# Performance work log

Measured on AMD Instinct MI355X. Metric: run time of the kernel, lower is better.

Reference implementation:

```python
import jax, jax.numpy as jnp
import numpy as np

HEADS = 8
FEATURE = 512
COMPUTE = 256
SEQ = 512
BATCH = 64


def setup_inputs() -> dict:
    key = jax.random.key(0)
    ks = jax.random.split(key, 10)
    d1 = jax.random.normal(ks[0], (BATCH, FEATURE), dtype=jnp.float32)
    d2 = jax.random.normal(ks[1], (SEQ, BATCH, FEATURE), dtype=jnp.float32)
    # linear1: Linear(FEATURE -> COMPUTE) + ReLU
    w1 = jax.random.normal(ks[2], (FEATURE, COMPUTE), dtype=jnp.float32) * (1.0 / np.sqrt(FEATURE))
    b1 = jnp.zeros((COMPUTE,), dtype=jnp.float32)
    # per-head score params, stacked: ws[i] is [2C, C], ps[i] is [C, 1]
    W = jax.random.normal(ks[3], (HEADS, 2 * COMPUTE, COMPUTE), dtype=jnp.float32)
    P = jax.random.normal(ks[4], (HEADS, COMPUTE), dtype=jnp.float32)
    # value projection weight_v: [FEATURE, COMPUTE]
    wv = jax.random.normal(ks[5], (FEATURE, COMPUTE), dtype=jnp.float32)
    # cc: Linear(COMPUTE*HEADS -> 128) + ReLU
    wcc = jax.random.normal(ks[6], (COMPUTE * HEADS, 128), dtype=jnp.float32) * (1.0 / np.sqrt(COMPUTE * HEADS))
    bcc = jnp.zeros((128,), dtype=jnp.float32)
    return {"d1": d1, "d2": d2, "w1": w1, "b1": b1, "W": W, "P": P,
            "wv": wv, "wcc": wcc, "bcc": bcc, "d2_size": SEQ}


def reference(d1, d2, w1, b1, W, P, wv, wcc, bcc, d2_size):
    S, B, F = d2.shape
    # linear1 on flattened d2 rows -> [S*B, C]
    d3 = jax.nn.relu(d2.reshape(-1, F) @ w1 + b1)
    # linear1 on d1, tiled S times along batch axis -> [S*B, C]
    d4 = jax.nn.relu(d1 @ w1 + b1)            # [B, C]
    d4 = jnp.tile(d4, (S, 1))                  # [S*B, C]
    d5 = jnp.concatenate([d3, d4], axis=1).reshape(S, B, -1)  # [S, B, 2C]
    # value path: tanh(d2 @ weight_v) -> [B, S, C]
    tv = jnp.tanh(jnp.einsum('sbf,fc->sbc', d2, wv)).transpose(1, 0, 2)
    # all heads batched: us = tanh(d5 @ W_h) -> [H, S, B, C]
    us = jnp.tanh(jnp.einsum('sbd,hdc->hsbc', d5, W))
    atts = jnp.einsum('hsbc,hc->hbs', us, P)   # [H, B, S]
    scores = jax.nn.softmax(atts, axis=-1)     # softmax over sequence
    vs = jnp.einsum('hbs,bsc->hbc', scores, tv)  # weighted sum over S -> [H, B, C]
    # torch.cat(vs, dim=1): head-major concat -> [B, H*C]
    vs = vs.transpose(1, 0, 2).reshape(B, -1)
    return jax.nn.relu(vs @ wcc + bcc)         # [B, 128]
```

## Files before the change

kernel.cpp:

```cpp
#include <hip/hip_runtime.h>
#include <cstddef>
#include <cstdint>

#define HH 8
#define FF 512
#define CC 256
#define SS 512
#define BB 64
#define SB (SS*BB)

typedef __attribute__((ext_vector_type(4))) float f32x4;
typedef __attribute__((ext_vector_type(8))) short bf16x8;

typedef __attribute__((address_space(1))) unsigned int gu32_t;
typedef __attribute__((address_space(3))) unsigned int lu32_t;

__device__ __forceinline__ void gld16(const void* gp, void* lp) {
    __builtin_amdgcn_global_load_lds((gu32_t*)gp, (lu32_t*)lp, 16, 0, 0);
}

__device__ __forceinline__ float fast_tanh(float x) {
    float e = __expf(2.0f * x);
    return 1.0f - 2.0f / (e + 1.0f);
}
__device__ __forceinline__ float relu_f(float x) { return fmaxf(x, 0.0f); }

__device__ __forceinline__ unsigned short f2bf(float x) {
    unsigned u = __float_as_uint(x);
    unsigned r = u + 0x7FFFu + ((u >> 16) & 1u);
    return (unsigned short)(r >> 16);
}
__device__ __forceinline__ float bf2f(unsigned short h) {
    return __uint_as_float(((unsigned)h) << 16);
}


__global__ __launch_bounds__(256) void p_prep(
    const float* __restrict__ w1, const float* __restrict__ wv,
    const float* __restrict__ W, const float* __restrict__ d1,
    const float* __restrict__ b1,
    unsigned short* __restrict__ w1ts, unsigned short* __restrict__ wvts,
    unsigned short* __restrict__ Wts, float* __restrict__ d4)
{
    __shared__ float T[64][65];
    __shared__ float As[16][68];
    __shared__ float Bs[16][68];
    const int tid = threadIdx.x;
    const int bid = blockIdx.x;
    if (bid < 192) {
        const float* src;
        unsigned short* dst;
        int kt64, nt;
        if (bid < 64) {
            int m = bid >> 5;
            int t = bid & 31;
            kt64 = t >> 2; nt = t & 3;
            src = m ? wv : w1;
            dst = m ? wvts : w1ts;
        } else {
            int t = bid - 64;
            int h = t >> 4; int tt = t & 15;
            kt64 = tt >> 2; nt = tt & 3;
            src = W + (size_t)h * 2 * CC * CC;
            dst = Wts + (size_t)h * 8 * CC * 64;
        }
        const int k0 = kt64 * 64, n0 = nt * 64;
        #pragma unroll
        for (int jj = 0; jj < 4; ++jj) {
            int i = (tid >> 4) + jj * 16;
            int j = (tid & 15) * 4;
            float4 v = *(const float4*)(src + (size_t)(k0 + i) * CC + n0 + j);
            T[i][j] = v.x; T[i][j+1] = v.y; T[i][j+2] = v.z; T[i][j+3] = v.w;
        }
        __syncthreads();
        {
            const int n_local = tid & 63;
            const int kg = (tid >> 6) * 16;
            const int n_abs = n0 + n_local;
            const int sxn = n_abs & 7;
            #pragma unroll
            for (int j = 0; j < 2; ++j) {
                const int kbase = kg + j * 8;
                const int k_abs = k0 + kbase;
                const int kt = k_abs >> 5;
                const int g = (k_abs >> 3) & 3;
                bf16x8 hv8, lv8;
                #pragma unroll
                for (int q = 0; q < 8; ++q) {
                    float x = T[kbase + q][n_local];
                    unsigned short hx = f2bf(x);
                    hv8[q] = (short)hx;
                    lv8[q] = (short)f2bf(x - bf2f(hx));
                }
                size_t rowo = ((size_t)kt * CC + n_abs) * 64;
                *(bf16x8*)(dst + rowo + (size_t)((2*g + 0) ^ sxn) * 8) = hv8;
                *(bf16x8*)(dst + rowo + (size_t)((2*g + 1) ^ sxn) * 8) = lv8;
            }
        }
    } else {
        const int n0 = (bid - 192) * 64;
        const int tx = tid & 15, ty = tid >> 4;
        const int lm = tid >> 2, lk4 = (tid & 3) * 4;
        const int bk = tid >> 4, bn4 = (tid & 15) * 4;
        float acc[4][4] = {};
        for (int k0 = 0; k0 < FF; k0 += 16) {
            float4 a = *(const float4*)(d1 + (size_t)lm * FF + k0 + lk4);
            As[lk4+0][lm] = a.x; As[lk4+1][lm] = a.y;
            As[lk4+2][lm] = a.z; As[lk4+3][lm] = a.w;
            *(float4*)&Bs[bk][bn4] = *(const float4*)(w1 + (size_t)(k0+bk)*CC + n0 + bn4);
            __syncthreads();
            #pragma unroll
            for (int kk = 0; kk < 16; ++kk) {
                float4 a4 = *(const float4*)&As[kk][ty*4];
                float4 b4 = *(const float4*)&Bs[kk][tx*4];
                float av[4] = {a4.x, a4.y, a4.z, a4.w};
                float bv[4] = {b4.x, b4.y, b4.z, b4.w};
                #pragma unroll
                for (int i = 0; i < 4; ++i)
                    #pragma unroll
                    for (int j = 0; j < 4; ++j)
                        acc[i][j] = fmaf(av[i], bv[j], acc[i][j]);
            }
            __syncthreads();
        }
        #pragma unroll
        for (int i = 0; i < 4; ++i) {
            int row = ty*4 + i;
            #pragma unroll
            for (int j = 0; j < 4; ++j)
                d4[(size_t)row*CC + n0 + tx*4 + j] = relu_f(acc[i][j] + b1[n0 + tx*4 + j]);
        }
    }
}

__global__ __launch_bounds__(256, 2) void k1_main(
    const float* __restrict__ d2,
    const unsigned short* __restrict__ w1ts, const unsigned short* __restrict__ wvts,
    const float* __restrict__ b1,
    const float* __restrict__ d4, const float* __restrict__ W,
    unsigned short* __restrict__ d3s, unsigned short* __restrict__ tv,
    float* __restrict__ e4)
{
    __shared__ __align__(16) unsigned short SH[24576];
    unsigned short* const Abuf = SH;
    unsigned short* const Bbuf = SH + 8192;

    const int tid = threadIdx.x;
    const int bid = blockIdx.x;

    if (bid >= 512) {
        float (*As)[68] = (float(*)[68])&SH[0];
        float (*Bs)[68] = (float(*)[68])&SH[8192];
        const int idx = bid - 512;
        const int n0 = (idx & 3) * 64;
        const int h  = idx >> 2;
        const float* Wh = W + ((size_t)h * 2 * CC + CC) * CC;
        const int tx = tid & 15, ty = tid >> 4;
        const int lm = tid >> 2, lk4 = (tid & 3) * 4;
        const int bk = tid >> 4, bn4 = (tid & 15) * 4;
        float acc[4][4] = {};
        for (int k0 = 0; k0 < CC; k0 += 16) {
            float4 a = *(const float4*)(d4 + (size_t)lm * CC + k0 + lk4);
            As[lk4+0][lm] = a.x; As[lk4+1][lm] = a.y;
            As[lk4+2][lm] = a.z; As[lk4+3][lm] = a.w;
            *(float4*)&Bs[bk][bn4] = *(const float4*)(Wh + (size_t)(k0+bk)*CC + n0 + bn4);
            __syncthreads();
            #pragma unroll
            for (int kk = 0; kk < 16; ++kk) {
                float4 a4 = *(const float4*)&As[kk][ty*4];
                float4 b4 = *(const float4*)&Bs[kk][tx*4];
                float av[4] = {a4.x, a4.y, a4.z, a4.w};
                float bv[4] = {b4.x, b4.y, b4.z, b4.w};
                #pragma unroll
                for (int i = 0; i < 4; ++i)
                    #pragma unroll
                    for (int j = 0; j < 4; ++j)
                        acc[i][j] = fmaf(av[i], bv[j], acc[i][j]);
            }
            __syncthreads();
        }
        #pragma unroll
        for (int i = 0; i < 4; ++i) {
            int b = ty*4 + i;
            #pragma unroll
            for (int j = 0; j < 4; ++j)
                e4[((size_t)h*BB + b)*CC + n0 + tx*4 + j] = acc[i][j];
        }
        return;
    }

    const int cxcd = bid & 7;
    const int jd   = bid >> 3;
    const int path = jd & 1;
    const int xb   = (jd >> 1) * 8 + cxcd;
    const int r0   = xb * 128;
    const int lane = tid & 63, w = tid >> 6;
    const int rowgrp = w & 1, colgrp = w >> 1;
    const int cb = lane & 15, quad = lane >> 4;
    const unsigned short* BT = path ? wvts : w1ts;

    f32x4 acc[4][8];
    f32x4 zero = {0.0f, 0.0f, 0.0f, 0.0f};
    #pragma unroll
    for (int rt = 0; rt < 4; ++rt)
        #pragma unroll
        for (int ct = 0; ct < 8; ++ct) acc[rt][ct] = zero;

    const int ar = tid >> 1, ak = (tid & 1) * 16;
    const int arx = ar & 7;
    const int g0 = ak >> 3;
    const int phi = (2 * quad) ^ (cb & 7);

    for (int k0 = 0; k0 < FF; k0 += 32) {
        const int kt = k0 >> 5;
        {
            const unsigned short* Bsrc = BT + (size_t)kt * (CC * 64);
            #pragma unroll
            for (int i = 0; i < 8; ++i) {
                int chunk = i * 4 + w;
                gld16(Bsrc + (size_t)chunk * 512 + lane * 8, &Bbuf[chunk * 512]);
            }
        }
        {
            const float* s = d2 + (size_t)(r0 + ar) * FF + k0 + ak;
            float v[16];
            *(float4*)&v[0]  = *(const float4*)(s);
            *(float4*)&v[4]  = *(const float4*)(s + 4);
            *(float4*)&v[8]  = *(const float4*)(s + 8);
            *(float4*)&v[12] = *(const float4*)(s + 12);
            bf16x8 vh0, vh1, vl0, vl1;
            #pragma unroll
            for (int j = 0; j < 8; ++j) {
                unsigned short h = f2bf(v[j]);
                vh0[j] = (short)h; vl0[j] = (short)f2bf(v[j] - bf2f(h));
                unsigned short h2 = f2bf(v[j+8]);
                vh1[j] = (short)h2; vl1[j] = (short)f2bf(v[j+8] - bf2f(h2));
            }
            unsigned short* Ar = &Abuf[ar * 64];
            *(bf16x8*)&Ar[((2*g0 + 0) ^ arx) * 8] = vh0;
            *(bf16x8*)&Ar[((2*g0 + 1) ^ arx) * 8] = vl0;
            *(bf16x8*)&Ar[((2*g0 + 2) ^ arx) * 8] = vh1;
            *(bf16x8*)&Ar[((2*g0 + 3) ^ arx) * 8] = vl1;
        }
        __syncthreads();
        bf16x8 ahf[4], alf[4];
        #pragma unroll
        for (int rt = 0; rt < 4; ++rt) {
            const unsigned short* Arow = &Abuf[(rowgrp*64 + rt*16 + cb) * 64];
            ahf[rt] = *(const bf16x8*)&Arow[phi * 8];
            alf[rt] = *(const bf16x8*)&Arow[(phi ^ 1) * 8];
        }
        #pragma unroll
        for (int ct = 0; ct < 8; ++ct) {
            const unsigned short* Brow = &Bbuf[(colgrp*128 + ct*16 + cb) * 64];
            bf16x8 bh = *(const bf16x8*)&Brow[phi * 8];
            bf16x8 bl = *(const bf16x8*)&Brow[(phi ^ 1) * 8];
            #pragma unroll
            for (int rt = 0; rt < 4; ++rt) {
                acc[rt][ct] = __builtin_amdgcn_mfma_f32_16x16x32_bf16(ahf[rt], bh, acc[rt][ct], 0, 0, 0);
                acc[rt][ct] = __builtin_amdgcn_mfma_f32_16x16x32_bf16(ahf[rt], bl, acc[rt][ct], 0, 0, 0);
                acc[rt][ct] = __builtin_amdgcn_mfma_f32_16x16x32_bf16(alf[rt], bh, acc[rt][ct], 0, 0, 0);
            }
        }
        __syncthreads();
    }

    if (path == 0) {
        float bias[8];
        #pragma unroll
        for (int ct = 0; ct < 8; ++ct) bias[ct] = b1[colgrp*128 + ct*16 + cb];
        unsigned short* Lp = SH + colgrp * 9216;
        #pragma unroll
        for (int it = 0; it < 4; ++it) {
            __syncthreads();
            #pragma unroll
            for (int rt = 0; rt < 4; ++rt)
                #pragma unroll
                for (int r = 0; r < 4; ++r) {
                    int row = rowgrp*64 + rt*16 + quad*4 + r;
                    int sx = row & 7;
                    #pragma unroll
                    for (int t = 0; t < 2; ++t) {
                        float val = relu_f(acc[rt][2*it + t][r] + bias[2*it + t]);
                        unsigned short hx = f2bf(val);
                        unsigned short lx = f2bf(val - bf2f(hx));
                        int cl = t*16 + cb;
                        int g = cl >> 3, c7 = cl & 7;
                        Lp[row*72 + (((2*g + 0) ^ sx) << 3) + c7] = hx;
                        Lp[row*72 + (((2*g + 1) ^ sx) << 3) + c7] = lx;
                    }
                }
            __syncthreads();
            #pragma unroll
            for (int q = 0; q < 8; ++q) {
                int idx = q*256 + tid;
                int pp  = idx >> 10;
                int rc  = idx & 1023;
                int row = rc >> 3;
                int ch  = rc & 7;
                bf16x8 v = *(const bf16x8*)&SH[pp*9216 + row*72 + ch*8];
                unsigned short* dst = d3s + ((size_t)(pp*4 + it) * SB + r0 + row) * 64;
                *(bf16x8*)&dst[ch*8] = v;
            }
        }
    } else {
        unsigned short* Lp = SH + colgrp * 6144;
        #pragma unroll
        for (int it = 0; it < 4; ++it) {
            __syncthreads();
            #pragma unroll
            for (int rt = 0; rt < 4; ++rt)
                #pragma unroll
                for (int r = 0; r < 4; ++r) {
                    int row = rowgrp*64 + rt*16 + quad*4 + r;
                    #pragma unroll
                    for (int t = 0; t < 2; ++t) {
                        int cl = t*16 + cb;
                        Lp[row*48 + cl] = f2bf(fast_tanh(acc[rt][2*it + t][r]));
                    }
                }
            __syncthreads();
            #pragma unroll
            for (int q = 0; q < 4; ++q) {
                int idx = q*256 + tid;
                int pp  = idx >> 9;
                int rc  = idx & 511;
                int row = rc >> 2;
                int ch  = rc & 3;
                bf16x8 v = *(const bf16x8*)&SH[pp*6144 + row*48 + ch*8];
                unsigned short* dst = tv + (size_t)(r0 + row) * CC + (pp*4 + it)*32;
                *(bf16x8*)&dst[ch*8] = v;
            }
        }
    }
}

__global__ __launch_bounds__(256, 2) void k3_atts(
    const unsigned short* __restrict__ d3s, const unsigned short* __restrict__ Wts,
    const float* __restrict__ e4, const float* __restrict__ P,
    float* __restrict__ atts)
{
    __shared__ __align__(16) unsigned short Abuf[128 * 64];
    __shared__ __align__(16) unsigned short Bbuf[256 * 64];
    float (*red)[128] = (float(*)[128])&Abuf[0];

    const int tid = threadIdx.x;
    const int lane = tid & 63, w = tid >> 6;
    const int bid = blockIdx.x;
    const int cxcd = bid & 7;
    const int jj   = bid >> 3;
    const int h    = jj & 7;
    const int xb   = (jj >> 3) * 8 + cxcd;
    const int r0   = xb * 128;
    const int rowgrp = w & 1, colgrp = w >> 1;
    const int cb = lane & 15, quad = lane >> 4;
    const int phi = (2 * quad) ^ (cb & 7);

    const unsigned short* Wh = Wts + (size_t)h * (8 * CC * 64);

    f32x4 acc[4][8];
    f32x4 zero = {0.0f, 0.0f, 0.0f, 0.0f};
    #pragma unroll
    for (int rt = 0; rt < 4; ++rt)
        #pragma unroll
        for (int ct = 0; ct < 8; ++ct) acc[rt][ct] = zero;

    for (int kt = 0; kt < 8; ++kt) {
        {
            const unsigned short* Asrc = d3s + ((size_t)kt * SB + r0) * 64;
            #pragma unroll
            for (int i = 0; i < 4; ++i) {
                int chunk = i * 4 + w;
                gld16(Asrc + (size_t)chunk * 512 + lane * 8, &Abuf[chunk * 512]);
            }
        }
        {
            const unsigned short* Bsrc = Wh + (size_t)kt * (CC * 64);
            #pragma unroll
            for (int i = 0; i < 8; ++i) {
                int chunk = i * 4 + w;
                gld16(Bsrc + (size_t)chunk * 512 + lane * 8, &Bbuf[chunk * 512]);
            }
        }
        __syncthreads();
        bf16x8 ahf[4], alf[4];
        #pragma unroll
        for (int rt = 0; rt < 4; ++rt) {
            const unsigned short* Arow = &Abuf[(rowgrp*64 + rt*16 + cb) * 64];
            ahf[rt] = *(const bf16x8*)&Arow[phi * 8];
            alf[rt] = *(const bf16x8*)&Arow[(phi ^ 1) * 8];
        }
        #pragma unroll
        for (int ct = 0; ct < 8; ++ct) {
            const unsigned short* Brow = &Bbuf[(colgrp*128 + ct*16 + cb) * 64];
            bf16x8 bh = *(const bf16x8*)&Brow[phi * 8];
            bf16x8 bl = *(const bf16x8*)&Brow[(phi ^ 1) * 8];
            #pragma unroll
            for (int rt = 0; rt < 4; ++rt) {
                acc[rt][ct] = __builtin_amdgcn_mfma_f32_16x16x32_bf16(ahf[rt], bh, acc[rt][ct], 0, 0, 0);
                acc[rt][ct] = __builtin_amdgcn_mfma_f32_16x16x32_bf16(ahf[rt], bl, acc[rt][ct], 0, 0, 0);
                acc[rt][ct] = __builtin_amdgcn_mfma_f32_16x16x32_bf16(alf[rt], bh, acc[rt][ct], 0, 0, 0);
            }
        }
        __syncthreads();
    }
    float Pv[8];
    #pragma unroll
    for (int ct = 0; ct < 8; ++ct) Pv[ct] = P[(size_t)h * CC + colgrp*128 + ct*16 + cb];
    #pragma unroll
    for (int rt = 0; rt < 4; ++rt) {
        #pragma unroll
        for (int r = 0; r < 4; ++r) {
            int b = rt*16 + quad*4 + r;
            const float* e4p = e4 + ((size_t)h * BB + b) * CC + colgrp*128 + cb;
            float part = 0.0f;
            #pragma unroll
            for (int ct = 0; ct < 8; ++ct) {
                float u = acc[rt][ct][r] + e4p[ct*16];
                part = fmaf(Pv[ct], fast_tanh(u), part);
            }
            part += __shfl_xor(part, 1); part += __shfl_xor(part, 2);
            part += __shfl_xor(part, 4); part += __shfl_xor(part, 8);
            if (cb == 0) red[colgrp][rowgrp*64 + b] = part;
        }
    }
    __syncthreads();
    if (tid < 128) {
        float v = red[0][tid] + red[1][tid];
        int gr = r0 + tid;
        int s = gr >> 6, b = gr & 63;
        atts[((size_t)h * BB + b) * SS + s] = v;
    }
}

__global__ __launch_bounds__(256) void k456_out(
    const float* __restrict__ atts, const unsigned short* __restrict__ tv,
    const float* __restrict__ wcc, const float* __restrict__ bcc,
    float* __restrict__ out)
{
    __shared__ float sc[HH][SS];
    __shared__ float red[4][2048];
    const int b = blockIdx.x;
    const int tid = threadIdx.x;
    const int lane = tid & 63, w = tid >> 6;

    for (int i = tid; i < HH*SS; i += 256) {
        int h = i >> 9, s = i & 511;
        sc[h][s] = atts[((size_t)h*BB + b)*SS + s];
    }
    __syncthreads();
    #pragma unroll
    for (int t = 0; t < 2; ++t) {
        int hh = w*2 + t;
        float x[8];
        #pragma unroll
        for (int j = 0; j < 8; ++j) x[j] = sc[hh][j*64 + lane];
        float m = x[0];
        #pragma unroll
        for (int j = 1; j < 8; ++j) m = fmaxf(m, x[j]);
        #pragma unroll
        for (int d = 1; d < 64; d <<= 1) m = fmaxf(m, __shfl_xor(m, d));
        float sum = 0.0f;
        #pragma unroll
        for (int j = 0; j < 8; ++j) { x[j] = __expf(x[j] - m); sum += x[j]; }
        #pragma unroll
        for (int d = 1; d < 64; d <<= 1) sum += __shfl_xor(sum, d);
        float inv = 1.0f / sum;
        #pragma unroll
        for (int j = 0; j < 8; ++j) sc[hh][j*64 + lane] = x[j] * inv;
    }
    __syncthreads();
    {
        const int cl = tid & 63, stripe = tid >> 6;
        const int c0 = cl * 4;
        const unsigned short* tvb = tv + ((size_t)(stripe * 128) * BB + b) * CC + c0;
        float acc[HH][4] = {};
        for (int si = 0; si < 128; ++si) {
            uint2 u = *(const uint2*)(tvb + (size_t)si * BB * CC);
            float x0 = bf2f((unsigned short)(u.x));
            float x1 = bf2f((unsigned short)(u.x >> 16));
            float x2 = bf2f((unsigned short)(u.y));
            float x3 = bf2f((unsigned short)(u.y >> 16));
            int s = stripe * 128 + si;
            #pragma unroll
            for (int h = 0; h < HH; ++h) {
                float wgt = sc[h][s];
                acc[h][0] = fmaf(wgt, x0, acc[h][0]);
                acc[h][1] = fmaf(wgt, x1, acc[h][1]);
                acc[h][2] = fmaf(wgt, x2, acc[h][2]);
                acc[h][3] = fmaf(wgt, x3, acc[h][3]);
            }
        }
        #pragma unroll
        for (int h = 0; h < HH; ++h)
            #pragma unroll
            for (int j = 0; j < 4; ++j)
                red[stripe][h*256 + c0 + j] = acc[h][j];
    }
    __syncthreads();
    for (int i = tid; i < 2048; i += 256)
        red[0][i] = red[0][i] + red[1][i] + red[2][i] + red[3][i];
    __syncthreads();
    {
        const int n = tid & 127, half = tid >> 7;
        float o = 0.0f;
        const int kbase = half * 1024;
        for (int k = 0; k < 1024; ++k)
            o = fmaf(red[0][kbase + k], wcc[(size_t)(kbase + k) * 128 + n], o);
        float* r2 = &sc[0][0];
        r2[half * 128 + n] = o;
    }
    __syncthreads();
    if (tid < 128)
        out[(size_t)b * 128 + tid] = relu_f(sc[0][tid] + sc[0][128 + tid] + bcc[tid]);
}

extern "C" void kernel_launch(void* const* d_in, const int* in_sizes, int n_in,
                              void* d_out, int out_size, void* d_ws, size_t ws_size,
                              hipStream_t stream)
{
    (void)in_sizes; (void)n_in; (void)out_size; (void)ws_size;
    const float* d1  = (const float*)d_in[0];
    const float* d2  = (const float*)d_in[1];
    const float* w1  = (const float*)d_in[2];
    const float* b1  = (const float*)d_in[3];
    const float* W   = (const float*)d_in[4];
    const float* P   = (const float*)d_in[5];
    const float* wv  = (const float*)d_in[6];
    const float* wcc = (const float*)d_in[7];
    const float* bcc = (const float*)d_in[8];
    float* out = (float*)d_out;

    char* p = (char*)d_ws;
    unsigned short* d3s  = (unsigned short*)p; p += (size_t)8 * SB * 64 * 2;
    unsigned short* tv   = (unsigned short*)p; p += (size_t)SB * CC * 2;
    unsigned short* w1ts = (unsigned short*)p; p += (size_t)16 * CC * 64 * 2;
    unsigned short* wvts = (unsigned short*)p; p += (size_t)16 * CC * 64 * 2;
    unsigned short* Wts  = (unsigned short*)p; p += (size_t)HH * 8 * CC * 64 * 2;
    float* d4   = (float*)p;  p += (size_t)BB * CC * 4;
    float* e4   = (float*)p;  p += (size_t)HH * BB * CC * 4;
    float* atts = (float*)p;  p += (size_t)HH * BB * SS * 4;

    p_prep   <<<dim3(196),       256, 0, stream>>>(w1, wv, W, d1, b1,
                  w1ts, wvts, Wts, d4);
    k1_main  <<<dim3(544),       256, 0, stream>>>(d2, w1ts, wvts, b1, d4, W,
                  d3s, tv, e4);
    k3_atts  <<<dim3(2048),      256, 0, stream>>>(d3s, Wts, e4, P, atts);
    k456_out <<<dim3(BB),        256, 0, stream>>>(atts, tv, wcc, bcc, out);
}
```

Before: 357.8 us.

## Split final attention-weighted sum across sequence quarters into two kernels

The final kernel ran only 64 blocks, one per batch element, on a large GPU. It is now split into two kernels. k456a launches 256 blocks, each redoing the softmax and accumulating one quarter of the sequence into a partial buffer. k456b sums the four partials and applies the output linear layer. This raises parallelism on the tv read, at the cost of an extra launch, a workspace round-trip, and softmax computed four times redundantly.

After: 348.7 us. 2.6% less time.

```diff
diff --git a/kernel.cpp b/kernel.cpp
--- a/kernel.cpp
+++ b/kernel.cpp
@@ -433,14 +433,14 @@
     }
 }
 
-__global__ __launch_bounds__(256) void k456_out(
+__global__ __launch_bounds__(256) void k456a(
     const float* __restrict__ atts, const unsigned short* __restrict__ tv,
-    const float* __restrict__ wcc, const float* __restrict__ bcc,
-    float* __restrict__ out)
+    float* __restrict__ vsp)
 {
     __shared__ float sc[HH][SS];
     __shared__ float red[4][2048];
-    const int b = blockIdx.x;
+    const int bq = blockIdx.x;
+    const int b = bq >> 2, q = bq & 3;
     const int tid = threadIdx.x;
     const int lane = tid & 63, w = tid >> 6;
 
@@ -471,17 +471,17 @@
     }
     __syncthreads();
     {
-        const int cl = tid & 63, stripe = tid >> 6;
-        const int c0 = cl * 4;
-        const unsigned short* tvb = tv + ((size_t)(stripe * 128) * BB + b) * CC + c0;
+        const int c0 = lane * 4;
+        const int s0 = q*128 + w*32;
+        const unsigned short* tvb = tv + ((size_t)s0 * BB + b) * CC + c0;
         float acc[HH][4] = {};
-        for (int si = 0; si < 128; ++si) {
+        for (int si = 0; si < 32; ++si) {
             uint2 u = *(const uint2*)(tvb + (size_t)si * BB * CC);
             float x0 = bf2f((unsigned short)(u.x));
             float x1 = bf2f((unsigned short)(u.x >> 16));
             float x2 = bf2f((unsigned short)(u.y));
             float x3 = bf2f((unsigned short)(u.y >> 16));
-            int s = stripe * 128 + si;
+            int s = s0 + si;
             #pragma unroll
             for (int h = 0; h < HH; ++h) {
                 float wgt = sc[h][s];
@@ -495,24 +495,37 @@
         for (int h = 0; h < HH; ++h)
             #pragma unroll
             for (int j = 0; j < 4; ++j)
-                red[stripe][h*256 + c0 + j] = acc[h][j];
+                red[w][h*256 + c0 + j] = acc[h][j];
     }
     __syncthreads();
+    float* dst = vsp + ((size_t)b * 4 + q) * 2048;
     for (int i = tid; i < 2048; i += 256)
-        red[0][i] = red[0][i] + red[1][i] + red[2][i] + red[3][i];
+        dst[i] = red[0][i] + red[1][i] + red[2][i] + red[3][i];
+}
+
+__global__ __launch_bounds__(256) void k456b(
+    const float* __restrict__ vsp, const float* __restrict__ wcc,
+    const float* __restrict__ bcc, float* __restrict__ out)
+{
+    __shared__ float vs[2048];
+    __shared__ float tmp[256];
+    const int b = blockIdx.x;
+    const int tid = threadIdx.x;
+    const float* src = vsp + (size_t)b * 4 * 2048;
+    for (int i = tid; i < 2048; i += 256)
+        vs[i] = src[i] + src[2048 + i] + src[4096 + i] + src[6144 + i];
     __syncthreads();
     {
         const int n = tid & 127, half = tid >> 7;
         float o = 0.0f;
         const int kbase = half * 1024;
         for (int k = 0; k < 1024; ++k)
-            o = fmaf(red[0][kbase + k], wcc[(size_t)(kbase + k) * 128 + n], o);
-        float* r2 = &sc[0][0];
-        r2[half * 128 + n] = o;
+            o = fmaf(vs[kbase + k], wcc[(size_t)(kbase + k) * 128 + n], o);
+        tmp[half * 128 + n] = o;
     }
     __syncthreads();
     if (tid < 128)
-        out[(size_t)b * 128 + tid] = relu_f(sc[0][tid] + sc[0][128 + tid] + bcc[tid]);
+        out[(size_t)b * 128 + tid] = relu_f(tmp[tid] + tmp[128 + tid] + bcc[tid]);
 }
 
 extern "C" void kernel_launch(void* const* d_in, const int* in_sizes, int n_in,
@@ -540,11 +553,13 @@
     float* d4   = (float*)p;  p += (size_t)BB * CC * 4;
     float* e4   = (float*)p;  p += (size_t)HH * BB * CC * 4;
     float* atts = (float*)p;  p += (size_t)HH * BB * SS * 4;
+    float* vsp  = (float*)p;  p += (size_t)BB * 4 * 2048 * 4;
 
     p_prep   <<<dim3(196),       256, 0, stream>>>(w1, wv, W, d1, b1,
                   w1ts, wvts, Wts, d4);
     k1_main  <<<dim3(544),       256, 0, stream>>>(d2, w1ts, wvts, b1, d4, W,
                   d3s, tv, e4);
     k3_atts  <<<dim3(2048),      256, 0, stream>>>(d3s, Wts, e4, P, atts);
-    k456_out <<<dim3(BB),        256, 0, stream>>>(atts, tv, wcc, bcc, out);
-}
+    k456a    <<<dim3(256),       256, 0, stream>>>(atts, tv, vsp);
+    k456b    <<<dim3(BB),        256, 0, stream>>>(vsp, wcc, bcc, out);
+}
```
